# Optimization experiments

Hardware: AMD Instinct MI355X
Metric: run time of the kernel (lower is better)

The kernel has to match this reference:

```python
import jax, jax.numpy as jnp
import numpy as np

B, N, D_IN = 8, 2048, 512
H = 1024          # MLP hidden
D_EMB = 512       # embed output dim
D_ATTN = 256      # attn_layers[-1]; KQ MLP outputs 2*D_ATTN


def setup_inputs() -> dict:
    key = jax.random.key(0)
    ks = jax.random.split(key, 9)
    s = lambda fi, fo: (2.0 / (fi + fo)) ** 0.5
    return {
        "x": jax.random.normal(ks[0], (B, N, D_IN), dtype=jnp.float32),
        # embed MLP: Linear(D_IN,H), ReLU, Linear(H,D_EMB)  (weights stored [in,out])
        "We1": jax.random.normal(ks[1], (D_IN, H), dtype=jnp.float32) * s(D_IN, H),
        "be1": jnp.zeros((H,), dtype=jnp.float32),
        "We2": jax.random.normal(ks[2], (H, D_EMB), dtype=jnp.float32) * s(H, D_EMB),
        "be2": jnp.zeros((D_EMB,), dtype=jnp.float32),
        # KQ MLP: Linear(D_IN,H), ReLU, Linear(H, 2*D_ATTN)
        "Wk1": jax.random.normal(ks[3], (D_IN, H), dtype=jnp.float32) * s(D_IN, H),
        "bk1": jnp.zeros((H,), dtype=jnp.float32),
        "Wk2": jax.random.normal(ks[4], (H, 2 * D_ATTN), dtype=jnp.float32) * s(H, 2 * D_ATTN),
        "bk2": jnp.zeros((2 * D_ATTN,), dtype=jnp.float32),
    }


def reference(x, We1, be1, We2, be2, Wk1, bk1, Wk2, bk2):
    # embed MLP
    embs = jax.nn.relu(x @ We1 + be1) @ We2 + be2            # [B,N,D_EMB]
    # KQ MLP; chunk: first half K, second half Q
    kq = jax.nn.relu(x @ Wk1 + bk1) @ Wk2 + bk2              # [B,N,2*D_ATTN]
    K, Q = kq[..., :D_ATTN], kq[..., D_ATTN:]
    # unscaled attention: softmax(Q K^T) V
    scores = jnp.einsum("bqd,bkd->bqk", Q, K)                # [B,N,N]
    A = jax.nn.softmax(scores, axis=-1)
    return jnp.einsum("bqk,bkd->bqd", A, embs)               # [B,N,D_EMB]
```

## Files before the change

### kernel.cpp

```cpp
#include <hip/hip_runtime.h>
#include <stdint.h>

using fx4   = __attribute__((ext_vector_type(4))) float;
using half8 = __attribute__((ext_vector_type(8))) _Float16;

__device__ __forceinline__ ushort f2h(float x) {
  _Float16 h = (_Float16)x;
  union { _Float16 hv; ushort u; } v; v.hv = h;
  return v.u;
}

__device__ __forceinline__ void gload_lds16(const ushort* g, ushort* l) {
  __builtin_amdgcn_global_load_lds(
      (__attribute__((address_space(1))) const void*)g,
      (__attribute__((address_space(3))) void*)l, 16, 0, 0);
}

#define MFMA16(a, b, c) __builtin_amdgcn_mfma_f32_16x16x32_f16(a, b, c, 0, 0, 0)

__global__ __launch_bounds__(256)
void gemm_bt(const ushort* __restrict__ A, int lda, long long sA,
             const ushort* __restrict__ B, int ldb, long long sB,
             const float* __restrict__ bias,
             void* __restrict__ C, int ldc, long long sC,
             int K, int flags)
{
  __shared__ ushort As[128 * 32];
  __shared__ ushort Bs[128 * 32];
  const int z = blockIdx.z;
  A += (long long)z * sA;
  B += (long long)z * sB;
  const int tid  = threadIdx.x;
  const int lane = tid & 63;
  const int wave = tid >> 6;
  const int wm   = (wave >> 1) * 64;
  const int wn   = (wave & 1) * 64;
  const long long bm = (long long)blockIdx.y * 128;
  const long long bn = (long long)blockIdx.x * 128;

  const int srow = tid >> 2;
  const int skq  = (tid & 3) * 8;
  const ushort* a0 = A + (bm + srow) * lda + skq;
  const ushort* a1 = a0 + 64LL * lda;
  const ushort* b0 = B + (bn + srow) * ldb + skq;
  const ushort* b1 = b0 + 64LL * ldb;
  ushort* lA0 = &As[tid * 8];
  ushort* lA1 = &As[2048 + tid * 8];
  ushort* lB0 = &Bs[tid * 8];
  ushort* lB1 = &Bs[2048 + tid * 8];

  fx4 acc[4][4] = {};
  const ushort* ap = &As[(wm + (lane & 15)) * 32 + (lane >> 4) * 8];
  const ushort* bp = &Bs[(wn + (lane & 15)) * 32 + (lane >> 4) * 8];

  for (int k0 = 0; k0 < K; k0 += 32) {
    gload_lds16(a0, lA0);
    gload_lds16(a1, lA1);
    gload_lds16(b0, lB0);
    gload_lds16(b1, lB1);
    a0 += 32; a1 += 32; b0 += 32; b1 += 32;
    __syncthreads();
    half8 af[4], bv[4];
#pragma unroll
    for (int t = 0; t < 4; ++t) {
      af[t] = *(const half8*)(ap + t * 16 * 32);
      bv[t] = *(const half8*)(bp + t * 16 * 32);
    }
#pragma unroll
    for (int i = 0; i < 4; ++i)
#pragma unroll
      for (int j = 0; j < 4; ++j)
        acc[i][j] = MFMA16(af[i], bv[j], acc[i][j]);
    __syncthreads();
  }

  const int col0 = (int)bn + wn + (lane & 15);
  const int row0 = (int)bm + wm + ((lane >> 4) << 2);

  if (flags & 16) {
    ushort* Ch = (ushort*)C + (long long)z * sC;
#pragma unroll
    for (int j = 0; j < 4; ++j) {
      const int col = col0 + j * 16;
      const float bvv = bias ? bias[col] : 0.0f;
#pragma unroll
      for (int i = 0; i < 4; ++i) {
        const int row = row0 + i * 16;
        ushort4 o;
        o.x = f2h(acc[i][j][0] + bvv);
        o.y = f2h(acc[i][j][1] + bvv);
        o.z = f2h(acc[i][j][2] + bvv);
        o.w = f2h(acc[i][j][3] + bvv);
        *(ushort4*)(Ch + (long long)col * ldc + row) = o;
      }
    }
    return;
  }

  float*  Cf = (float*)C + (long long)z * sC;
  ushort* Ch = (ushort*)C + (long long)z * sC;
#pragma unroll
  for (int j = 0; j < 4; ++j) {
    const int col = col0 + j * 16;
    const float bvv = bias ? bias[col] : 0.0f;
#pragma unroll
    for (int i = 0; i < 4; ++i) {
      const long long row = row0 + i * 16;
#pragma unroll
      for (int r = 0; r < 4; ++r) {
        float v = acc[i][j][r] + bvv;
        if (flags & 1) v = fmaxf(v, 0.0f);
        if (flags & 2) Ch[(row + r) * ldc + col] = f2h(v);
        else           Cf[(row + r) * ldc + col] = v;
      }
    }
  }
}

__global__ __launch_bounds__(256, 2)
void attn_fused(const ushort* __restrict__ KQ, const ushort* __restrict__ EMBT,
                float* __restrict__ out)
{
  __shared__ ushort smem[40960];
  ushort* const Qs = smem;
  ushort* const U  = smem + 8192;

  const int tid  = threadIdx.x;
  const int lane = tid & 63;
  const int w    = tid >> 6;
  const int c    = lane & 15;
  const int q4   = lane >> 4;
  const int z    = blockIdx.x;
  const long long tb = (long long)z * 2048;
  const int q0   = blockIdx.y * 32;

#pragma unroll
  for (int p = 0; p < 4; ++p) {
    const int u = p * 256 + tid;
    const int panel = u >> 7, row = (u & 127) >> 2, kg = (u & 3) * 8;
    gload_lds16(KQ + (tb + q0 + row) * 512 + 256 + panel * 32 + kg, Qs + u * 8);
  }

  float lp[2][4] = {};
  for (int t0 = 0; t0 < 2048; t0 += 128) {
#pragma unroll
    for (int p = 0; p < 16; ++p) {
      const int u = p * 256 + tid;
      const int panel = u >> 9, row = (u & 511) >> 2, kg = (u & 3) * 8;
      gload_lds16(KQ + (tb + t0 + row) * 512 + panel * 32 + kg, U + u * 8);
    }
    __syncthreads();
    fx4 s[2][2] = {};
#pragma unroll
    for (int dc = 0; dc < 8; ++dc) {
      const half8 a0 = *(const half8*)(Qs + dc * 1024 + c * 32 + q4 * 8);
      const half8 a1 = *(const half8*)(Qs + dc * 1024 + (16 + c) * 32 + q4 * 8);
      const half8 b0 = *(const half8*)(U + dc * 4096 + (w * 32 + c) * 32 + q4 * 8);
      const half8 b1 = *(const half8*)(U + dc * 4096 + (w * 32 + 16 + c) * 32 + q4 * 8);
      s[0][0] = MFMA16(a0, b0, s[0][0]); s[0][1] = MFMA16(a0, b1, s[0][1]);
      s[1][0] = MFMA16(a1, b0, s[1][0]); s[1][1] = MFMA16(a1, b1, s[1][1]);
    }
#pragma unroll
    for (int i = 0; i < 2; ++i)
#pragma unroll
      for (int r = 0; r < 4; ++r)
        lp[i][r] += __expf(s[i][0][r] - 40.0f) + __expf(s[i][1][r] - 40.0f);
    __syncthreads();
  }
#pragma unroll
  for (int i = 0; i < 2; ++i)
#pragma unroll
    for (int r = 0; r < 4; ++r) {
      float v = lp[i][r];
      v += __shfl_xor(v, 1, 64); v += __shfl_xor(v, 2, 64);
      v += __shfl_xor(v, 4, 64); v += __shfl_xor(v, 8, 64);
      lp[i][r] = v;
    }
  float* l_lds = (float*)U;
  if (c == 0) {
#pragma unroll
    for (int i = 0; i < 2; ++i)
#pragma unroll
      for (int r = 0; r < 4; ++r)
        l_lds[w * 32 + i * 16 + q4 * 4 + r] = lp[i][r];
  }
  __syncthreads();
  float linv[2][4];
#pragma unroll
  for (int i = 0; i < 2; ++i)
#pragma unroll
    for (int r = 0; r < 4; ++r) {
      const int row = i * 16 + q4 * 4 + r;
      linv[i][r] = 1.0f / (l_lds[row] + l_lds[32 + row] + l_lds[64 + row] + l_lds[96 + row]);
    }
  __syncthreads();

  fx4 o[2][8] = {};
  for (int t0 = 0; t0 < 2048; t0 += 128) {
#pragma unroll
    for (int p = 0; p < 16; ++p) {
      const int u = p * 256 + tid;
      const int panel = u >> 9, row = (u & 511) >> 2, kg = (u & 3) * 8;
      gload_lds16(KQ + (tb + t0 + row) * 512 + panel * 32 + kg, U + u * 8);
    }
    __syncthreads();
    fx4 s[2][2] = {};
#pragma unroll
    for (int dc = 0; dc < 8; ++dc) {
      const half8 a0 = *(const half8*)(Qs + dc * 1024 + c * 32 + q4 * 8);
      const half8 a1 = *(const half8*)(Qs + dc * 1024 + (16 + c) * 32 + q4 * 8);
      const half8 b0 = *(const half8*)(U + dc * 4096 + (w * 32 + c) * 32 + q4 * 8);
      const half8 b1 = *(const half8*)(U + dc * 4096 + (w * 32 + 16 + c) * 32 + q4 * 8);
      s[0][0] = MFMA16(a0, b0, s[0][0]); s[0][1] = MFMA16(a0, b1, s[0][1]);
      s[1][0] = MFMA16(a1, b0, s[1][0]); s[1][1] = MFMA16(a1, b1, s[1][1]);
    }
    __syncthreads();
    ushort* Ps = U;
#pragma unroll
    for (int i = 0; i < 2; ++i)
#pragma unroll
      for (int j = 0; j < 2; ++j)
#pragma unroll
        for (int r = 0; r < 4; ++r)
          Ps[w * 1024 + (i * 16 + q4 * 4 + r) * 32 + j * 16 + c] =
              f2h(__expf(s[i][j][r] - 40.0f) * linv[i][r]);
    __syncthreads();
    ushort* Vs = U + 4096;
    for (int kc = 0; kc < 4; ++kc) {
#pragma unroll
      for (int p = 0; p < 8; ++p) {
        const int u = p * 256 + tid;
        const int d = u >> 2, tg = (u & 3) * 8;
        gload_lds16(EMBT + (long long)d * 16384 + tb + t0 + kc * 32 + tg, Vs + u * 8);
      }
      __syncthreads();
      const half8 pa0 = *(const half8*)(Ps + kc * 1024 + c * 32 + q4 * 8);
      const half8 pa1 = *(const half8*)(Ps + kc * 1024 + (16 + c) * 32 + q4 * 8);
#pragma unroll
      for (int j = 0; j < 8; ++j) {
        const half8 vb = *(const half8*)(Vs + (w * 128 + j * 16 + c) * 32 + q4 * 8);
        o[0][j] = MFMA16(pa0, vb, o[0][j]);
        o[1][j] = MFMA16(pa1, vb, o[1][j]);
      }
      __syncthreads();
    }
  }

  float* ob = out + (tb + q0) * 512;
#pragma unroll
  for (int i = 0; i < 2; ++i)
#pragma unroll
    for (int r = 0; r < 4; ++r) {
      const int row = i * 16 + q4 * 4 + r;
#pragma unroll
      for (int j = 0; j < 8; ++j)
        ob[(long long)row * 512 + w * 128 + j * 16 + c] = o[i][j][r];
    }
}

__global__ __launch_bounds__(256)
void transpose_cast_w(const float* __restrict__ in, ushort* __restrict__ out, int R, int C) {
  __shared__ float tile[32][33];
  const int c0 = blockIdx.x * 32, r0 = blockIdx.y * 32;
  const int tx = threadIdx.x & 31, ty = threadIdx.x >> 5;
#pragma unroll
  for (int i = 0; i < 32; i += 8)
    tile[ty + i][tx] = in[(long long)(r0 + ty + i) * C + (c0 + tx)];
  __syncthreads();
#pragma unroll
  for (int i = 0; i < 32; i += 8)
    out[(long long)(c0 + ty + i) * R + (r0 + tx)] = f2h(tile[tx][ty + i]);
}

__global__ __launch_bounds__(256)
void cast_f32_f16(const float* __restrict__ in, ushort* __restrict__ out) {
  const long long i = ((long long)blockIdx.x * 256 + threadIdx.x) * 4;
  const float4 v = *(const float4*)(in + i);
  ushort4 o;
  o.x = f2h(v.x); o.y = f2h(v.y); o.z = f2h(v.z); o.w = f2h(v.w);
  *(ushort4*)(out + i) = o;
}

__global__ __launch_bounds__(256)
void concat_bias(const float* __restrict__ b0, const float* __restrict__ b1,
                 float* __restrict__ out) {
  const int i = blockIdx.x * 256 + threadIdx.x;
  out[i] = (i < 1024) ? b0[i] : b1[i - 1024];
}

extern "C" void kernel_launch(void* const* d_in, const int* in_sizes, int n_in,
                              void* d_out, int out_size, void* d_ws, size_t ws_size,
                              hipStream_t stream) {
  (void)in_sizes; (void)n_in; (void)out_size; (void)ws_size;
  const float* x   = (const float*)d_in[0];
  const float* We1 = (const float*)d_in[1];
  const float* be1 = (const float*)d_in[2];
  const float* We2 = (const float*)d_in[3];
  const float* be2 = (const float*)d_in[4];
  const float* Wk1 = (const float*)d_in[5];
  const float* bk1 = (const float*)d_in[6];
  const float* Wk2 = (const float*)d_in[7];
  const float* bk2 = (const float*)d_in[8];
  float* out = (float*)d_out;
  char* ws = (char*)d_ws;

  ushort* Xb   = (ushort*)(ws + 0);
  ushort* W2c  = (ushort*)(ws + 0);
  ushort* H    = (ushort*)(ws + 16777216);
  ushort* EMBT = (ushort*)(ws + 83886080);
  ushort* KQ   = (ushort*)(ws + 100663296);
  float*  b1c  = (float*)(ws + 117440512);
  ushort* W1c  = (ushort*)(ws + 117448704);

  cast_f32_f16<<<dim3(8192), 256, 0, stream>>>(x, Xb);
  transpose_cast_w<<<dim3(32, 16), 256, 0, stream>>>(We1, W1c, 512, 1024);
  transpose_cast_w<<<dim3(32, 16), 256, 0, stream>>>(Wk1, W1c + 524288, 512, 1024);
  concat_bias<<<dim3(8), 256, 0, stream>>>(be1, bk1, b1c);

  gemm_bt<<<dim3(16, 128, 1), 256, 0, stream>>>(Xb, 512, 0, W1c, 512, 0, b1c,
                                                H, 2048, 0, 512, 1 | 2);

  transpose_cast_w<<<dim3(16, 32), 256, 0, stream>>>(We2, W2c, 1024, 512);
  transpose_cast_w<<<dim3(16, 32), 256, 0, stream>>>(Wk2, W2c + 524288, 1024, 512);

  gemm_bt<<<dim3(4, 128, 1), 256, 0, stream>>>(H, 2048, 0, W2c, 1024, 0, be2,
                                               EMBT, 16384, 0, 1024, 16);
  gemm_bt<<<dim3(4, 128, 1), 256, 0, stream>>>(H + 1024, 2048, 0, W2c + 524288, 1024, 0, bk2,
                                               KQ, 512, 0, 1024, 2);

  attn_fused<<<dim3(8, 64), 256, 0, stream>>>(KQ, EMBT, out);
}
```

Measured before the change: 378.6 us.

## Replace two-pass fixed-offset softmax attention with single-pass online softmax

The attention kernel previously ran two passes over all keys: one to accumulate softmax denominators with a fixed exponent offset, and a second to recompute scores and multiply by V. It now uses a single pass with online softmax (running row max, alpha rescaling of accumulators), halving the QK^T work and K reads. It also moves to 512-thread blocks covering 64 queries, and reads K and V fragments straight from global memory instead of staging them in LDS. Extra block-wide syncs per tile for the max reduction and uncoalesced direct global loads could offset the savings.

```diff
diff --git a/kernel.cpp b/kernel.cpp
--- a/kernel.cpp
+++ b/kernel.cpp
@@ -117,144 +117,154 @@
   }
 }
 
-__global__ __launch_bounds__(256, 2)
+__global__ __launch_bounds__(512, 2)
 void attn_fused(const ushort* __restrict__ KQ, const ushort* __restrict__ EMBT,
                 float* __restrict__ out)
 {
-  __shared__ ushort smem[40960];
-  ushort* const Qs = smem;
-  ushort* const U  = smem + 8192;
+  __shared__ ushort Qs[20480];
+  __shared__ ushort Ps[10240];
+  __shared__ float  rmax[256];
+  __shared__ float  mstate[64];
+  __shared__ float  mnewA[64];
+  __shared__ float  alphaA[64];
+  __shared__ float  lred[256];
 
   const int tid  = threadIdx.x;
   const int lane = tid & 63;
   const int w    = tid >> 6;
   const int c    = lane & 15;
   const int q4   = lane >> 4;
+  const int qw   = w >> 2;
+  const int tw   = w & 3;
+  const int dw   = w * 64;
   const int z    = blockIdx.x;
   const long long tb = (long long)z * 2048;
-  const int q0   = blockIdx.y * 32;
+  const int q0   = blockIdx.y * 64;
 
 #pragma unroll
   for (int p = 0; p < 4; ++p) {
-    const int u = p * 256 + tid;
-    const int panel = u >> 7, row = (u & 127) >> 2, kg = (u & 3) * 8;
-    gload_lds16(KQ + (tb + q0 + row) * 512 + 256 + panel * 32 + kg, Qs + u * 8);
-  }
-
-  float lp[2][4] = {};
+    const int cu  = p * 512 + tid;
+    const int row = cu >> 5;
+    const int kch = cu & 31;
+    const int dc  = kch >> 2, qg = kch & 3;
+    const half8 v = *(const half8*)(KQ + (tb + q0 + row) * 512 + 256 + dc * 32 + qg * 8);
+    *(half8*)(Qs + dc * 2560 + row * 40 + qg * 8) = v;
+  }
+  if (tid < 64) mstate[tid] = -3.0e38f;
+  __syncthreads();
+
+  float l_part[2][4] = {};
+  fx4 o[4][4] = {};
+
   for (int t0 = 0; t0 < 2048; t0 += 128) {
-#pragma unroll
-    for (int p = 0; p < 16; ++p) {
-      const int u = p * 256 + tid;
-      const int panel = u >> 9, row = (u & 511) >> 2, kg = (u & 3) * 8;
-      gload_lds16(KQ + (tb + t0 + row) * 512 + panel * 32 + kg, U + u * 8);
-    }
-    __syncthreads();
     fx4 s[2][2] = {};
+    const ushort* kb0 = KQ + (tb + t0 + tw * 32 + c) * 512;
+    const ushort* kb1 = kb0 + 16 * 512;
 #pragma unroll
     for (int dc = 0; dc < 8; ++dc) {
-      const half8 a0 = *(const half8*)(Qs + dc * 1024 + c * 32 + q4 * 8);
-      const half8 a1 = *(const half8*)(Qs + dc * 1024 + (16 + c) * 32 + q4 * 8);
-      const half8 b0 = *(const half8*)(U + dc * 4096 + (w * 32 + c) * 32 + q4 * 8);
-      const half8 b1 = *(const half8*)(U + dc * 4096 + (w * 32 + 16 + c) * 32 + q4 * 8);
+      const half8 a0 = *(const half8*)(Qs + dc * 2560 + (qw * 32 + c) * 40 + q4 * 8);
+      const half8 a1 = *(const half8*)(Qs + dc * 2560 + (qw * 32 + 16 + c) * 40 + q4 * 8);
+      const half8 b0 = *(const half8*)(kb0 + dc * 32 + q4 * 8);
+      const half8 b1 = *(const half8*)(kb1 + dc * 32 + q4 * 8);
       s[0][0] = MFMA16(a0, b0, s[0][0]); s[0][1] = MFMA16(a0, b1, s[0][1]);
       s[1][0] = MFMA16(a1, b0, s[1][0]); s[1][1] = MFMA16(a1, b1, s[1][1]);
     }
 #pragma unroll
+    for (int i = 0; i < 2; ++i) {
+      fx4 rm;
+#pragma unroll
+      for (int r = 0; r < 4; ++r) rm[r] = fmaxf(s[i][0][r], s[i][1][r]);
+#pragma unroll
+      for (int off = 1; off < 16; off <<= 1)
+#pragma unroll
+        for (int r = 0; r < 4; ++r) rm[r] = fmaxf(rm[r], __shfl_xor(rm[r], off, 64));
+      if (c == 0) {
+#pragma unroll
+        for (int r = 0; r < 4; ++r)
+          rmax[tw * 64 + qw * 32 + i * 16 + q4 * 4 + r] = rm[r];
+      }
+    }
+    __syncthreads();
+    if (w == 0) {
+      const float mo = mstate[lane];
+      float mn = fmaxf(fmaxf(rmax[lane], rmax[64 + lane]),
+                       fmaxf(rmax[128 + lane], rmax[192 + lane]));
+      mn = fmaxf(mn, mo);
+      mnewA[lane]  = mn;
+      alphaA[lane] = __expf(mo - mn);
+      mstate[lane] = mn;
+    }
+    __syncthreads();
+#pragma unroll
     for (int i = 0; i < 2; ++i)
 #pragma unroll
+      for (int r = 0; r < 4; ++r) {
+        const int q = qw * 32 + i * 16 + q4 * 4 + r;
+        const float mn = mnewA[q];
+        const float e0 = __expf(s[i][0][r] - mn);
+        const float e1 = __expf(s[i][1][r] - mn);
+        l_part[i][r] = alphaA[q] * l_part[i][r] + e0 + e1;
+        Ps[tw * 2560 + q * 40 + c]      = f2h(e0);
+        Ps[tw * 2560 + q * 40 + 16 + c] = f2h(e1);
+      }
+#pragma unroll
+    for (int i4 = 0; i4 < 4; ++i4)
+#pragma unroll
+      for (int r = 0; r < 4; ++r) {
+        const float aq = alphaA[i4 * 16 + q4 * 4 + r];
+#pragma unroll
+        for (int n = 0; n < 4; ++n) o[i4][n][r] *= aq;
+      }
+    __syncthreads();
+#pragma unroll
+    for (int kc = 0; kc < 4; ++kc) {
+      half8 vb[4];
+#pragma unroll
+      for (int n = 0; n < 4; ++n)
+        vb[n] = *(const half8*)(EMBT + (long long)(dw + n * 16 + c) * 16384 +
+                                tb + t0 + kc * 32 + q4 * 8);
+      half8 pa[4];
+#pragma unroll
+      for (int i4 = 0; i4 < 4; ++i4)
+        pa[i4] = *(const half8*)(Ps + kc * 2560 + (i4 * 16 + c) * 40 + q4 * 8);
+#pragma unroll
+      for (int i4 = 0; i4 < 4; ++i4)
+#pragma unroll
+        for (int n = 0; n < 4; ++n)
+          o[i4][n] = MFMA16(pa[i4], vb[n], o[i4][n]);
+    }
+  }
+
+#pragma unroll
+  for (int i = 0; i < 2; ++i) {
+    fx4 lv;
+#pragma unroll
+    for (int r = 0; r < 4; ++r) lv[r] = l_part[i][r];
+#pragma unroll
+    for (int off = 1; off < 16; off <<= 1)
+#pragma unroll
+      for (int r = 0; r < 4; ++r) lv[r] += __shfl_xor(lv[r], off, 64);
+    if (c == 0) {
+#pragma unroll
       for (int r = 0; r < 4; ++r)
-        lp[i][r] += __expf(s[i][0][r] - 40.0f) + __expf(s[i][1][r] - 40.0f);
-    __syncthreads();
-  }
-#pragma unroll
-  for (int i = 0; i < 2; ++i)
+        lred[tw * 64 + qw * 32 + i * 16 + q4 * 4 + r] = lv[r];
+    }
+  }
+  __syncthreads();
+  if (w == 0)
+    alphaA[lane] = 1.0f / (lred[lane] + lred[64 + lane] + lred[128 + lane] + lred[192 + lane]);
+  __syncthreads();
+
+  float* ob = out + (tb + q0) * 512 + dw;
+#pragma unroll
+  for (int i4 = 0; i4 < 4; ++i4)
 #pragma unroll
     for (int r = 0; r < 4; ++r) {
-      float v = lp[i][r];
-      v += __shfl_xor(v, 1, 64); v += __shfl_xor(v, 2, 64);
-      v += __shfl_xor(v, 4, 64); v += __shfl_xor(v, 8, 64);
-      lp[i][r] = v;
-    }
-  float* l_lds = (float*)U;
-  if (c == 0) {
-#pragma unroll
-    for (int i = 0; i < 2; ++i)
-#pragma unroll
-      for (int r = 0; r < 4; ++r)
-        l_lds[w * 32 + i * 16 + q4 * 4 + r] = lp[i][r];
-  }
-  __syncthreads();
-  float linv[2][4];
-#pragma unroll
-  for (int i = 0; i < 2; ++i)
-#pragma unroll
-    for (int r = 0; r < 4; ++r) {
-      const int row = i * 16 + q4 * 4 + r;
-      linv[i][r] = 1.0f / (l_lds[row] + l_lds[32 + row] + l_lds[64 + row] + l_lds[96 + row]);
-    }
-  __syncthreads();
-
-  fx4 o[2][8] = {};
-  for (int t0 = 0; t0 < 2048; t0 += 128) {
-#pragma unroll
-    for (int p = 0; p < 16; ++p) {
-      const int u = p * 256 + tid;
-      const int panel = u >> 9, row = (u & 511) >> 2, kg = (u & 3) * 8;
-      gload_lds16(KQ + (tb + t0 + row) * 512 + panel * 32 + kg, U + u * 8);
-    }
-    __syncthreads();
-    fx4 s[2][2] = {};
-#pragma unroll
-    for (int dc = 0; dc < 8; ++dc) {
-      const half8 a0 = *(const half8*)(Qs + dc * 1024 + c * 32 + q4 * 8);
-      const half8 a1 = *(const half8*)(Qs + dc * 1024 + (16 + c) * 32 + q4 * 8);
-      const half8 b0 = *(const half8*)(U + dc * 4096 + (w * 32 + c) * 32 + q4 * 8);
-      const half8 b1 = *(const half8*)(U + dc * 4096 + (w * 32 + 16 + c) * 32 + q4 * 8);
-      s[0][0] = MFMA16(a0, b0, s[0][0]); s[0][1] = MFMA16(a0, b1, s[0][1]);
-      s[1][0] = MFMA16(a1, b0, s[1][0]); s[1][1] = MFMA16(a1, b1, s[1][1]);
-    }
-    __syncthreads();
-    ushort* Ps = U;
-#pragma unroll
-    for (int i = 0; i < 2; ++i)
-#pragma unroll
-      for (int j = 0; j < 2; ++j)
-#pragma unroll
-        for (int r = 0; r < 4; ++r)
-          Ps[w * 1024 + (i * 16 + q4 * 4 + r) * 32 + j * 16 + c] =
-              f2h(__expf(s[i][j][r] - 40.0f) * linv[i][r]);
-    __syncthreads();
-    ushort* Vs = U + 4096;
-    for (int kc = 0; kc < 4; ++kc) {
-#pragma unroll
-      for (int p = 0; p < 8; ++p) {
-        const int u = p * 256 + tid;
-        const int d = u >> 2, tg = (u & 3) * 8;
-        gload_lds16(EMBT + (long long)d * 16384 + tb + t0 + kc * 32 + tg, Vs + u * 8);
-      }
-      __syncthreads();
-      const half8 pa0 = *(const half8*)(Ps + kc * 1024 + c * 32 + q4 * 8);
-      const half8 pa1 = *(const half8*)(Ps + kc * 1024 + (16 + c) * 32 + q4 * 8);
-#pragma unroll
-      for (int j = 0; j < 8; ++j) {
-        const half8 vb = *(const half8*)(Vs + (w * 128 + j * 16 + c) * 32 + q4 * 8);
-        o[0][j] = MFMA16(pa0, vb, o[0][j]);
-        o[1][j] = MFMA16(pa1, vb, o[1][j]);
-      }
-      __syncthreads();
-    }
-  }
-
-  float* ob = out + (tb + q0) * 512;
-#pragma unroll
-  for (int i = 0; i < 2; ++i)
-#pragma unroll
-    for (int r = 0; r < 4; ++r) {
-      const int row = i * 16 + q4 * 4 + r;
-#pragma unroll
-      for (int j = 0; j < 8; ++j)
-        ob[(long long)row * 512 + w * 128 + j * 16 + c] = o[i][j][r];
+      const int q = i4 * 16 + q4 * 4 + r;
+      const float li = alphaA[q];
+#pragma unroll
+      for (int n = 0; n < 4; ++n)
+        ob[(long long)q * 512 + n * 16 + c] = o[i4][n][r] * li;
     }
 }
 
@@ -328,5 +338,5 @@
   gemm_bt<<<dim3(4, 128, 1), 256, 0, stream>>>(H + 1024, 2048, 0, W2c + 524288, 1024, 0, bk2,
                                                KQ, 512, 0, 1024, 2);
 
-  attn_fused<<<dim3(8, 64), 256, 0, stream>>>(KQ, EMBT, out);
-}
+  attn_fused<<<dim3(8, 32), 512, 0, stream>>>(KQ, EMBT, out);
+}
```

Result: slower. 390.8 us (+3.2%).
